# Optimization experiments

Hardware: AMD Instinct MI355X
Metric: run time of the kernel (lower is better)

The kernel has to match this reference:

```python
import jax, jax.numpy as jnp
import numpy as np

MIN_, MAX_, KSZ, IGNORE_IDX = 10, 10, 3, -255
B, H, W = 256, 256, 256
LI_MAX_ITERS = 64


def setup_inputs() -> dict:
    key = jax.random.key(0)
    x = jax.random.uniform(key, (B, 1, H, W), dtype=jnp.float32)
    return {"x": x}


def _otsu(hist):
    # hist: [256] counts. Returns Otsu threshold (bin value); fg = img > t.
    bins = jnp.arange(256, dtype=jnp.float32)
    w0 = jnp.cumsum(hist)[:-1]
    w1 = hist.sum() - w0
    s0 = jnp.cumsum(hist * bins)[:-1]
    s_tot = (hist * bins).sum()
    m0 = s0 / jnp.maximum(w0, 1e-12)
    m1 = (s_tot - s0) / jnp.maximum(w1, 1e-12)
    var_b = w0 * w1 * (m0 - m1) ** 2
    return jnp.argmax(var_b).astype(jnp.float32)


def _li(hist, init_t):
    # Histogram-based Li iterative minimum cross-entropy threshold
    # (skimage.filters.threshold_li with initial_guess=init_t).
    bins = jnp.arange(256, dtype=jnp.float32)
    img_min = jnp.min(jnp.where(hist > 0, bins, 255.0))
    vals = bins - img_min  # shift so values >= 0 (as skimage does)
    csum = jnp.cumsum(hist)
    cvsum = jnp.cumsum(hist * vals)
    n_tot, s_tot = csum[-1], cvsum[-1]
    tol = 0.5  # integer image -> half the minimal value spacing

    def body(state):
        t_curr, _, i = state
        # background: img <= t_curr + img_min
        idx = jnp.clip(jnp.floor(t_curr + img_min).astype(jnp.int32), 0, 255)
        n_back, s_back = csum[idx], cvsum[idx]
        n_fore, s_fore = n_tot - n_back, s_tot - s_back
        mean_back = jnp.where(n_back > 0, s_back / jnp.maximum(n_back, 1.0), 0.0)
        mean_fore = s_fore / jnp.maximum(n_fore, 1.0)
        eps = 1e-12
        t_next = (mean_back - mean_fore) / (
            jnp.log(jnp.maximum(mean_back, eps)) - jnp.log(jnp.maximum(mean_fore, eps)))
        t_next = jnp.where(mean_back < eps, mean_fore / 2.0, t_next)
        return (t_next, t_curr, i + 1)

    def cond(state):
        t_curr, t_prev, i = state
        return (jnp.abs(t_curr - t_prev) > tol) & (i < LI_MAX_ITERS)

    t0 = init_t - img_min
    t_fin, _, _ = jax.lax.while_loop(cond, body, (t0, t0 + 10.0, 0))
    return t_fin + img_min


def _sample_mask(key, region, k):
    # Uniform sampling without replacement of up to k pixels from region
    # (bool [H,W]) via random-score top-k (equiv. to torch.multinomial
    # with uniform probs, w/o replacement).
    flat = region.reshape(-1)
    scores = jnp.where(flat, jax.random.uniform(key, (flat.shape[0],)), -1.0)
    top, idx = jax.lax.top_k(scores, k)
    valid = (top >= 0.0).astype(jnp.int32)
    mask = jnp.zeros(flat.shape[0], jnp.int32).at[idx].max(valid)
    return mask.reshape(region.shape)


def _dilate(m):
    # kornia dilation with ones (KSZ,KSZ) kernel on a 0/1 mask == max filter.
    return jax.lax.reduce_window(m, 0, jax.lax.max, (KSZ, KSZ), (1, 1), "SAME")


def _per_image(img_u8, key_fg, key_bg):
    # img_u8: [H,W] int32 in [0,255]
    hist = jnp.zeros(256, jnp.float32).at[img_u8.ravel()].add(1.0)
    otsu = jnp.clip(_otsu(hist), 1.0, 254.0)  # clamp 0->1, 255->254
    li_t = _li(hist, otsu)
    roi = img_u8.astype(jnp.float32) > li_t

    fg = _sample_mask(key_fg, roi, MAX_)
    bg = _sample_mask(key_bg, jnp.logical_not(roi), MIN_)
    if KSZ > 1:
        fg = _dilate(fg)
        bg = _dilate(bg)

    overlap = (fg + bg) == 2
    fg = jnp.where(overlap, 0, fg)
    bg = jnp.where(overlap, 0, bg)

    seeds = jnp.full((H, W), IGNORE_IDX, jnp.int32)
    seeds = jnp.where(bg == 1, 0, seeds)
    seeds = jnp.where(fg == 1, 1, seeds)
    return seeds


def reference(x):
    b = x.shape[0]
    # (cam*255).astype(uint8): truncation, cam in [0,1]
    img = jnp.clip(jnp.floor(x[:, 0] * 255.0), 0, 255).astype(jnp.int32)
    keys = jax.random.split(jax.random.key(1), (b, 2))
    return jax.vmap(_per_image)(img, keys[:, 0], keys[:, 1])
```

## Files before the change

### kernel.cpp

```cpp
#include <hip/hip_runtime.h>
#include <stdint.h>

#define NPIX 65536
#define IGN (-255)
#define CAP 768

__device__ __forceinline__ uint32_t rotl32(uint32_t v, uint32_t r){ return (v<<r)|(v>>(32u-r)); }

__device__ __forceinline__ void tf2x32(uint32_t k0, uint32_t k1, uint32_t x0, uint32_t x1,
                                       uint32_t &o0, uint32_t &o1){
  uint32_t k2 = k0 ^ k1 ^ 0x1BD11BDAu;
  x0 += k0; x1 += k1;
#define TFR(r) { x0 += x1; x1 = rotl32(x1,(r)); x1 ^= x0; }
  TFR(13u) TFR(15u) TFR(26u) TFR(6u)   x0 += k1; x1 += k2 + 1u;
  TFR(17u) TFR(29u) TFR(16u) TFR(24u)  x0 += k2; x1 += k0 + 2u;
  TFR(13u) TFR(15u) TFR(26u) TFR(6u)   x0 += k0; x1 += k1 + 3u;
  TFR(17u) TFR(29u) TFR(16u) TFR(24u)  x0 += k1; x1 += k2 + 4u;
  TFR(13u) TFR(15u) TFR(26u) TFR(6u)   x0 += k2; x1 += k0 + 5u;
#undef TFR
  o0 = x0; o1 = x1;
}

__device__ __forceinline__ unsigned long long packCand(uint32_t bits, uint32_t pix){
  float f = __uint_as_float((bits >> 9) | 0x3f800000u) - 1.0f;
  uint32_t u = __float_as_uint(f) ^ 0x80000000u;
  return ((unsigned long long)u << 32) | (unsigned long long)(0xFFFFFFFFu - pix);
}

__device__ __forceinline__ void t10_insert(unsigned long long* l, unsigned long long c){
  if (c > l[9]) {
    l[9] = c;
#pragma unroll
    for (int i = 9; i > 0; --i){
      unsigned long long a = l[i-1], b2 = l[i];
      if (b2 > a){ l[i-1] = b2; l[i] = a; }
    }
  }
}

__global__ __launch_bounds__(1024, 4)
void apm_kernel(const float* __restrict__ x, int* __restrict__ out){
  const int b = blockIdx.x;
  const int tid = threadIdx.x;
  const float* img = x + (size_t)b * NPIX;
  int* outb = out + (size_t)b * NPIX;

  __shared__ uint32_t hist[256];
  __shared__ float csum[256], cvsum[256];
  __shared__ unsigned long long buf[2][CAP];
  __shared__ uint32_t s_kw[4];
  __shared__ int s_cnt[2];
  __shared__ int s_nroi;
  __shared__ int s_imin;
  __shared__ unsigned long long s_best;
  __shared__ float s_lit;
  __shared__ int s_fail[2];
  __shared__ int s_pr[2][10], s_pc[2][10], s_np[2];

  if (tid < 256) hist[tid] = 0u;
  if (tid == 0){ s_cnt[0] = 0; s_cnt[1] = 0; s_nroi = 0; s_imin = 255; s_best = 0ull; }
  if (tid < 2){
    uint32_t o0, o1;
    tf2x32(0u, 1u, 0u, (uint32_t)(2*b + tid), o0, o1);
    s_kw[2*tid] = o0; s_kw[2*tid+1] = o1;
  }
  __syncthreads();

  uint32_t packed[16];
  {
    int4 f4 = make_int4(IGN, IGN, IGN, IGN);
    const float4* x4 = (const float4*)img;
    int4* o4 = (int4*)outb;
#pragma unroll
    for (int j = 0; j < 16; ++j){
      int p4 = tid + 1024*j;
      float4 v = x4[p4];
      o4[p4] = f4;
      uint32_t u0 = (uint32_t)min(max((int)floorf(v.x*255.0f),0),255);
      uint32_t u1 = (uint32_t)min(max((int)floorf(v.y*255.0f),0),255);
      uint32_t u2 = (uint32_t)min(max((int)floorf(v.z*255.0f),0),255);
      uint32_t u3 = (uint32_t)min(max((int)floorf(v.w*255.0f),0),255);
      packed[j] = u0 | (u1<<8) | (u2<<16) | (u3<<24);
      atomicAdd(&hist[u0],1u); atomicAdd(&hist[u1],1u);
      atomicAdd(&hist[u2],1u); atomicAdd(&hist[u3],1u);
    }
  }
  __syncthreads();

  if (tid < 256 && hist[tid]) atomicMin(&s_imin, tid);
  __syncthreads();
  const float img_min = (float)s_imin;

  if (tid < 256){
    float h = (float)hist[tid];
    csum[tid]  = h;
    cvsum[tid] = h * ((float)tid - img_min);
  }
  __syncthreads();
  for (int off = 1; off < 256; off <<= 1){
    float a = 0.f, c2 = 0.f;
    if (tid < 256 && tid >= off){ a = csum[tid-off]; c2 = cvsum[tid-off]; }
    __syncthreads();
    if (tid < 256 && tid >= off){ csum[tid] += a; cvsum[tid] += c2; }
    __syncthreads();
  }

  {
    float s_tot_o = cvsum[255] + img_min * csum[255];
    if (tid < 255){
      float w0 = csum[tid];
      float w1 = 65536.0f - w0;
      float cs = cvsum[tid] + img_min * csum[tid];
      float m0 = cs / fmaxf(w0, 1e-12f);
      float m1 = (s_tot_o - cs) / fmaxf(w1, 1e-12f);
      float d = m0 - m1;
      float vb = (w0*w1) * (d*d);
      unsigned long long pk =
        ((unsigned long long)__float_as_uint(vb) << 32) | (unsigned long long)(255 - tid);
      atomicMax(&s_best, pk);
    }
  }
  __syncthreads();

  if (tid == 0){
    int bestIdx = 255 - (int)(s_best & 0xFFFFFFFFull);
    float otsu = fminf(fmaxf((float)bestIdx, 1.0f), 254.0f);
    float n_tot = csum[255], s_tot = cvsum[255];
    float t_curr = otsu - img_min, t_prev = t_curr + 10.0f;
    int it = 0;
    while (fabsf(t_curr - t_prev) > 0.5f && it < 64){
      int idx = min(max((int)floorf(t_curr + img_min), 0), 255);
      float n_back = csum[idx], s_back = cvsum[idx];
      float n_fore = n_tot - n_back, s_fore = s_tot - s_back;
      float mean_back = (n_back > 0.0f) ? (s_back / fmaxf(n_back, 1.0f)) : 0.0f;
      float mean_fore = s_fore / fmaxf(n_fore, 1.0f);
      float t_next = (mean_back - mean_fore) /
                     (logf(fmaxf(mean_back, 1e-12f)) - logf(fmaxf(mean_fore, 1e-12f)));
      if (mean_back < 1e-12f) t_next = mean_fore * 0.5f;
      t_prev = t_curr; t_curr = t_next; ++it;
    }
    s_lit = t_curr + img_min;
  }
  __syncthreads();

  const float lit = s_lit;
  const uint32_t fk0 = s_kw[0], fk1 = s_kw[1], bk0 = s_kw[2], bk1 = s_kw[3];
  const uint32_t THRM = (0xFF000000u >> 9);
  int my_roi = 0;
#pragma unroll
  for (int j = 0; j < 16; ++j){
    uint32_t pk = packed[j];
    uint32_t pix0 = (uint32_t)(4*(tid + 1024*j));
#pragma unroll
    for (int s = 0; s < 4; ++s){
      uint32_t q = (pk >> (8*s)) & 255u;
      bool r = ((float)q > lit);
      my_roi += r ? 1 : 0;
      uint32_t o0, o1;
      tf2x32(r ? fk0 : bk0, r ? fk1 : bk1, 0u, pix0 + (uint32_t)s, o0, o1);
      uint32_t bits = o0 ^ o1;
      if ((bits >> 9) >= THRM){
        int r2 = r ? 0 : 1;
        int idx = atomicAdd(&s_cnt[r2], 1);
        if (idx < CAP) buf[r2][idx] = packCand(bits, pix0 + (uint32_t)s);
      }
    }
  }
  for (int off = 32; off; off >>= 1) my_roi += __shfl_down(my_roi, off);
  if ((tid & 63) == 0) atomicAdd(&s_nroi, my_roi);
  __syncthreads();

  if (tid == 0){
    int m0r = s_nroi, m1r = NPIX - s_nroi;
    int c0 = s_cnt[0], c1 = s_cnt[1];
    s_fail[0] = (c0 > CAP) || (c0 < 10 && c0 != m0r);
    s_fail[1] = (c1 > CAP) || (c1 < 10 && c1 != m1r);
  }
  __syncthreads();

  if (s_fail[0] || s_fail[1]){
    if (tid < 64){
      for (int r2 = 0; r2 < 2; ++r2){
        if (!s_fail[r2]) continue;
        uint32_t kk0 = s_kw[2*r2], kk1 = s_kw[2*r2+1];
        unsigned long long t[10];
#pragma unroll
        for (int i = 0; i < 10; ++i) t[i] = 0ull;
        for (int k2 = 0; k2 < 1024; ++k2){
          uint32_t pix = (uint32_t)(tid + 64*k2);
          float v = img[pix];
          int q = min(max((int)floorf(v*255.0f),0),255);
          bool r = ((float)q > lit);
          if (r != (r2 == 0)) continue;
          uint32_t o0, o1; tf2x32(kk0, kk1, 0u, pix, o0, o1);
          t10_insert(t, packCand(o0 ^ o1, pix));
        }
#pragma unroll
        for (int i = 0; i < 10; ++i) buf[r2][tid*10 + i] = t[i];
      }
    }
    __syncthreads();
    if (tid < 2 && s_fail[tid]){
      unsigned long long t[10];
#pragma unroll
      for (int i = 0; i < 10; ++i) t[i] = 0ull;
      for (int i = 0; i < 640; ++i) t10_insert(t, buf[tid][i]);
#pragma unroll
      for (int i = 0; i < 10; ++i) buf[tid][i] = t[i];
      s_cnt[tid] = 10;
    }
    __syncthreads();
  }

  if (tid == 0 || tid == 64){
    int r2 = (tid == 0) ? 0 : 1;
    int n = min(s_cnt[r2], CAP);
    unsigned long long t[10];
#pragma unroll
    for (int i = 0; i < 10; ++i) t[i] = 0ull;
    for (int i = 0; i < n; ++i) t10_insert(t, buf[r2][i]);
    int np = 0;
    for (int i = 0; i < 10; ++i){
      if (t[i]){
        uint32_t pix = 0xFFFFFFFFu - (uint32_t)(t[i] & 0xFFFFFFFFull);
        s_pr[r2][np] = (int)(pix >> 8);
        s_pc[r2][np] = (int)(pix & 255u);
        ++np;
      }
    }
    s_np[r2] = np;
  }
  __syncthreads();

  const int nfg = s_np[0], nbg = s_np[1];
  const int npts = nfg + nbg;
  if (tid < npts*9){
    int k = tid / 9, d = tid - k*9;
    int pr = (k < nfg) ? s_pr[0][k] : s_pr[1][k - nfg];
    int pc = (k < nfg) ? s_pc[0][k] : s_pc[1][k - nfg];
    pr += d/3 - 1; pc += d%3 - 1;
    if (pr >= 0 && pr < 256 && pc >= 0 && pc < 256){
      bool fgd = false, bgd = false;
      for (int i = 0; i < nfg; ++i) fgd |= (abs(pr - s_pr[0][i]) <= 1) && (abs(pc - s_pc[0][i]) <= 1);
      for (int i = 0; i < nbg; ++i) bgd |= (abs(pr - s_pr[1][i]) <= 1) && (abs(pc - s_pc[1][i]) <= 1);
      int val = (fgd && bgd) ? IGN : (fgd ? 1 : 0);
      outb[pr*256 + pc] = val;
    }
  }
}

extern "C" void kernel_launch(void* const* d_in, const int* in_sizes, int n_in,
                              void* d_out, int out_size, void* d_ws, size_t ws_size,
                              hipStream_t stream) {
  const float* x = (const float*)d_in[0];
  int* out = (int*)d_out;
  int B = in_sizes[0] / NPIX;
  apm_kernel<<<B, 1024, 0, stream>>>(x, out);
}
```

Baseline: 177.8 us.

## Split per-image kernel into four launches with sub-image blocks and scratch in output

Replaces the single 1024-thread-per-image kernel with four kernels: a partial-histogram pass over eighths of each image (with 4-way replicated shared histograms), a per-image threshold kernel, a per-eighth Threefry scoring pass that appends candidate pixels to global memory, and a final per-image selection/dilation kernel. The output buffer doubles as scratch for partial histograms and metadata, and is reset to the ignore value at the end. This spreads the bandwidth- and ALU-heavy passes over 8x more blocks for better occupancy. The cost is reading the input twice, extra launches, and global atomics on the candidate counters.

```diff
diff --git a/kernel.cpp b/kernel.cpp
--- a/kernel.cpp
+++ b/kernel.cpp
@@ -3,7 +3,13 @@
 
 #define NPIX 65536
 #define IGN (-255)
-#define CAP 768
+#define CAP 1022
+#define META_LI   2048
+#define META_CF   2049
+#define META_CB   2050
+#define META_NROI 2051
+#define META_FG   2052
+#define META_BG   3074
 
 __device__ __forceinline__ uint32_t rotl32(uint32_t v, uint32_t r){ return (v<<r)|(v>>(32u-r)); }
 
@@ -38,70 +44,65 @@
   }
 }
 
-__global__ __launch_bounds__(1024, 4)
-void apm_kernel(const float* __restrict__ x, int* __restrict__ out){
+__global__ __launch_bounds__(256, 8)
+void ka_hist_fill(const float* __restrict__ x, int* __restrict__ out){
+  const int blk = blockIdx.x;
+  const int b = blk >> 3, j8 = blk & 7;
+  const int tid = threadIdx.x;
+  const float4* x4 = (const float4*)(x + (size_t)b * NPIX) + j8 * 2048;
+  int4* o4 = (int4*)(out + (size_t)b * NPIX) + j8 * 2048;
+
+  __shared__ uint32_t histR[1024];
+#pragma unroll
+  for (int k = 0; k < 4; ++k) histR[tid + 256*k] = 0u;
+  __syncthreads();
+
+  const int4 f4 = make_int4(IGN, IGN, IGN, IGN);
+  const uint32_t c4 = (uint32_t)(tid & 3);
+#pragma unroll
+  for (int jj = 0; jj < 8; ++jj){
+    int p4 = tid + 256*jj;
+    float4 v = x4[p4];
+    if (j8 != 0 || jj >= 4) o4[p4] = f4;
+    uint32_t u0 = (uint32_t)min(max((int)floorf(v.x*255.0f),0),255);
+    uint32_t u1 = (uint32_t)min(max((int)floorf(v.y*255.0f),0),255);
+    uint32_t u2 = (uint32_t)min(max((int)floorf(v.z*255.0f),0),255);
+    uint32_t u3 = (uint32_t)min(max((int)floorf(v.w*255.0f),0),255);
+    atomicAdd(&histR[(u0<<2)|c4],1u); atomicAdd(&histR[(u1<<2)|c4],1u);
+    atomicAdd(&histR[(u2<<2)|c4],1u); atomicAdd(&histR[(u3<<2)|c4],1u);
+  }
+  __syncthreads();
+  uint32_t s = histR[4*tid] + histR[4*tid+1] + histR[4*tid+2] + histR[4*tid+3];
+  out[(size_t)b*NPIX + j8*256 + tid] = (int)s;
+}
+
+__global__ __launch_bounds__(256, 2)
+void kb_thresh(int* __restrict__ out){
   const int b = blockIdx.x;
   const int tid = threadIdx.x;
-  const float* img = x + (size_t)b * NPIX;
-  int* outb = out + (size_t)b * NPIX;
-
-  __shared__ uint32_t hist[256];
+  int* meta = out + (size_t)b * NPIX;
+
   __shared__ float csum[256], cvsum[256];
-  __shared__ unsigned long long buf[2][CAP];
-  __shared__ uint32_t s_kw[4];
-  __shared__ int s_cnt[2];
-  __shared__ int s_nroi;
   __shared__ int s_imin;
   __shared__ unsigned long long s_best;
-  __shared__ float s_lit;
-  __shared__ int s_fail[2];
-  __shared__ int s_pr[2][10], s_pc[2][10], s_np[2];
-
-  if (tid < 256) hist[tid] = 0u;
-  if (tid == 0){ s_cnt[0] = 0; s_cnt[1] = 0; s_nroi = 0; s_imin = 255; s_best = 0ull; }
-  if (tid < 2){
-    uint32_t o0, o1;
-    tf2x32(0u, 1u, 0u, (uint32_t)(2*b + tid), o0, o1);
-    s_kw[2*tid] = o0; s_kw[2*tid+1] = o1;
-  }
-  __syncthreads();
-
-  uint32_t packed[16];
-  {
-    int4 f4 = make_int4(IGN, IGN, IGN, IGN);
-    const float4* x4 = (const float4*)img;
-    int4* o4 = (int4*)outb;
-#pragma unroll
-    for (int j = 0; j < 16; ++j){
-      int p4 = tid + 1024*j;
-      float4 v = x4[p4];
-      o4[p4] = f4;
-      uint32_t u0 = (uint32_t)min(max((int)floorf(v.x*255.0f),0),255);
-      uint32_t u1 = (uint32_t)min(max((int)floorf(v.y*255.0f),0),255);
-      uint32_t u2 = (uint32_t)min(max((int)floorf(v.z*255.0f),0),255);
-      uint32_t u3 = (uint32_t)min(max((int)floorf(v.w*255.0f),0),255);
-      packed[j] = u0 | (u1<<8) | (u2<<16) | (u3<<24);
-      atomicAdd(&hist[u0],1u); atomicAdd(&hist[u1],1u);
-      atomicAdd(&hist[u2],1u); atomicAdd(&hist[u3],1u);
-    }
-  }
-  __syncthreads();
-
-  if (tid < 256 && hist[tid]) atomicMin(&s_imin, tid);
+  if (tid == 0){ s_imin = 255; s_best = 0ull; }
+  __syncthreads();
+
+  int h = 0;
+#pragma unroll
+  for (int j = 0; j < 8; ++j) h += meta[j*256 + tid];
+  if (h) atomicMin(&s_imin, tid);
   __syncthreads();
   const float img_min = (float)s_imin;
 
-  if (tid < 256){
-    float h = (float)hist[tid];
-    csum[tid]  = h;
-    cvsum[tid] = h * ((float)tid - img_min);
-  }
+  csum[tid]  = (float)h;
+  cvsum[tid] = (float)h * ((float)tid - img_min);
   __syncthreads();
   for (int off = 1; off < 256; off <<= 1){
     float a = 0.f, c2 = 0.f;
-    if (tid < 256 && tid >= off){ a = csum[tid-off]; c2 = cvsum[tid-off]; }
+    if (tid >= off){ a = csum[tid-off]; c2 = cvsum[tid-off]; }
     __syncthreads();
-    if (tid < 256 && tid >= off){ csum[tid] += a; cvsum[tid] += c2; }
+    if (tid >= off){ csum[tid] += a; cvsum[tid] += c2; }
     __syncthreads();
   }
 
@@ -139,45 +140,105 @@
       if (mean_back < 1e-12f) t_next = mean_fore * 0.5f;
       t_prev = t_curr; t_curr = t_next; ++it;
     }
-    s_lit = t_curr + img_min;
-  }
+    float lit = t_curr + img_min;
+    meta[META_LI] = __float_as_int(lit);
+    int idx = min(max((int)floorf(lit), 0), 255);
+    meta[META_NROI] = NPIX - (int)csum[idx];
+    meta[META_CF] = 0;
+    meta[META_CB] = 0;
+  }
+}
+
+__global__ __launch_bounds__(256, 4)
+void kc_score(const float* __restrict__ x, int* __restrict__ out){
+  const int blk = blockIdx.x;
+  const int b = blk >> 3, j8 = blk & 7;
+  const int tid = threadIdx.x;
+  int* meta = out + (size_t)b * NPIX;
+  const float4* x4 = (const float4*)(x + (size_t)b * NPIX) + j8 * 2048;
+
+  __shared__ uint32_t s_kw[4];
+  __shared__ float s_lit;
+  if (tid < 2){
+    uint32_t o0, o1;
+    tf2x32(0u, 1u, 0u, (uint32_t)(2*b + tid), o0, o1);
+    s_kw[2*tid] = o0; s_kw[2*tid+1] = o1;
+  }
+  if (tid == 0) s_lit = __int_as_float(meta[META_LI]);
   __syncthreads();
 
   const float lit = s_lit;
   const uint32_t fk0 = s_kw[0], fk1 = s_kw[1], bk0 = s_kw[2], bk1 = s_kw[3];
   const uint32_t THRM = (0xFF000000u >> 9);
-  int my_roi = 0;
-#pragma unroll
-  for (int j = 0; j < 16; ++j){
-    uint32_t pk = packed[j];
-    uint32_t pix0 = (uint32_t)(4*(tid + 1024*j));
+#pragma unroll
+  for (int jj = 0; jj < 8; ++jj){
+    int p4 = tid + 256*jj;
+    float4 v = x4[p4];
+    uint32_t u0 = (uint32_t)min(max((int)floorf(v.x*255.0f),0),255);
+    uint32_t u1 = (uint32_t)min(max((int)floorf(v.y*255.0f),0),255);
+    uint32_t u2 = (uint32_t)min(max((int)floorf(v.z*255.0f),0),255);
+    uint32_t u3 = (uint32_t)min(max((int)floorf(v.w*255.0f),0),255);
+    uint32_t pk = u0 | (u1<<8) | (u2<<16) | (u3<<24);
+    uint32_t pix0 = (uint32_t)(j8*8192 + 4*p4);
 #pragma unroll
     for (int s = 0; s < 4; ++s){
       uint32_t q = (pk >> (8*s)) & 255u;
       bool r = ((float)q > lit);
-      my_roi += r ? 1 : 0;
       uint32_t o0, o1;
       tf2x32(r ? fk0 : bk0, r ? fk1 : bk1, 0u, pix0 + (uint32_t)s, o0, o1);
       uint32_t bits = o0 ^ o1;
       if ((bits >> 9) >= THRM){
         int r2 = r ? 0 : 1;
-        int idx = atomicAdd(&s_cnt[r2], 1);
-        if (idx < CAP) buf[r2][idx] = packCand(bits, pix0 + (uint32_t)s);
+        int idx = atomicAdd(&meta[META_CF + r2], 1);
+        if (idx < CAP) meta[(r2 ? META_BG : META_FG) + idx] = (int)(pix0 + (uint32_t)s);
       }
     }
   }
-  for (int off = 32; off; off >>= 1) my_roi += __shfl_down(my_roi, off);
-  if ((tid & 63) == 0) atomicAdd(&s_nroi, my_roi);
-  __syncthreads();
-
+}
+
+__global__ __launch_bounds__(1024, 4)
+void kd_final(const float* __restrict__ x, int* __restrict__ out){
+  const int b = blockIdx.x;
+  const int tid = threadIdx.x;
+  int* meta = out + (size_t)b * NPIX;
+  int* outb = meta;
+  const float* img = x + (size_t)b * NPIX;
+
+  __shared__ unsigned long long buf[2][CAP];
+  __shared__ uint32_t s_kw[4];
+  __shared__ int s_cnt[2], s_fail[2], s_np[2];
+  __shared__ float s_lit;
+  __shared__ int s_pr[2][10], s_pc[2][10];
+
+  if (tid < 2){
+    uint32_t o0, o1;
+    tf2x32(0u, 1u, 0u, (uint32_t)(2*b + tid), o0, o1);
+    s_kw[2*tid] = o0; s_kw[2*tid+1] = o1;
+  }
   if (tid == 0){
-    int m0r = s_nroi, m1r = NPIX - s_nroi;
-    int c0 = s_cnt[0], c1 = s_cnt[1];
+    s_lit = __int_as_float(meta[META_LI]);
+    int c0 = meta[META_CF], c1 = meta[META_CB];
+    int nroi = meta[META_NROI];
+    s_cnt[0] = c0; s_cnt[1] = c1;
+    int m0r = nroi, m1r = NPIX - nroi;
     s_fail[0] = (c0 > CAP) || (c0 < 10 && c0 != m0r);
     s_fail[1] = (c1 > CAP) || (c1 < 10 && c1 != m1r);
   }
   __syncthreads();
 
+  {
+    int r2 = tid >> 9, lane = tid & 511;
+    uint32_t kk0 = s_kw[2*r2], kk1 = s_kw[2*r2+1];
+    int n = min(s_cnt[r2], CAP);
+    for (int i = lane; i < n; i += 512){
+      uint32_t pix = (uint32_t)meta[(r2 ? META_BG : META_FG) + i];
+      uint32_t o0, o1; tf2x32(kk0, kk1, 0u, pix, o0, o1);
+      buf[r2][i] = packCand(o0 ^ o1, pix);
+    }
+  }
+  __syncthreads();
+
+  const float lit = s_lit;
   if (s_fail[0] || s_fail[1]){
     if (tid < 64){
       for (int r2 = 0; r2 < 2; ++r2){
@@ -230,6 +291,9 @@
     }
     s_np[r2] = np;
   }
+  __syncthreads();
+
+  ((int4*)meta)[tid] = make_int4(IGN, IGN, IGN, IGN);
   __syncthreads();
 
   const int nfg = s_np[0], nbg = s_np[1];
@@ -255,5 +319,8 @@
   const float* x = (const float*)d_in[0];
   int* out = (int*)d_out;
   int B = in_sizes[0] / NPIX;
-  apm_kernel<<<B, 1024, 0, stream>>>(x, out);
-}
+  ka_hist_fill<<<8*B, 256, 0, stream>>>(x, out);
+  kb_thresh  <<<B,   256, 0, stream>>>(out);
+  kc_score   <<<8*B, 256, 0, stream>>>(x, out);
+  kd_final   <<<B,  1024, 0, stream>>>(x, out);
+}
```

After: 193.7 us. 1.09x slower.
